# Kernel tuning notes

Hardware: AMD Instinct MI355X
Metric: run time of the kernel (lower is better)

## Reference

```python
import jax, jax.numpy as jnp
import numpy as np

N, E, IN, ED, H, HID, OUT, G = 50000, 800000, 128, 16, 4, 64, 128, 64
NEG_SLOPE = 0.2


def _glorot(key, shape):
    fan_in, fan_out = shape[0], shape[-1]
    lim = float(np.sqrt(6.0 / (fan_in + fan_out)))
    return jax.random.uniform(key, shape, jnp.float32, -lim, lim)


def setup_inputs() -> dict:
    key = jax.random.key(0)
    ks = jax.random.split(key, 32)
    inp = {}
    inp['x'] = jax.random.normal(ks[0], (N, IN), jnp.float32)
    inp['edge_index'] = jax.random.randint(ks[1], (2, E), 0, N)
    inp['edge_attr'] = jax.random.normal(ks[2], (E, ED), jnp.float32)
    inp['batch'] = jnp.sort(jax.random.randint(ks[3], (N,), 0, G))
    # layer dims: (in_channels, out_channels_per_head, concat)
    dims = [(IN, HID, True), (H * HID, HID, True), (H * HID, OUT, False)]
    k = 4
    for i, (cin, c, concat) in enumerate(dims):
        inp[f'W{i}'] = _glorot(ks[k], (cin, H * c)); k += 1
        inp[f'asrc{i}'] = _glorot(ks[k], (1, H, c)); k += 1
        inp[f'adst{i}'] = _glorot(ks[k], (1, H, c)); k += 1
        inp[f'We{i}'] = _glorot(ks[k], (ED, H * c)); k += 1
        inp[f'ae{i}'] = _glorot(ks[k], (1, H, c)); k += 1
        inp[f'b{i}'] = jnp.zeros((H * c if concat else c,), jnp.float32); k += 1
    return inp


def _gat_layer(x, src, dst, ea, W, asrc, adst, We, ae, b, c, concat):
    # PyG GATConv math (eval mode, shared lin for src/dst, edge_dim set).
    n = x.shape[0]
    h = (x @ W).reshape(n, H, c)                      # [N,H,C]
    a_s = (h * asrc).sum(-1)                          # [N,H]
    a_d = (h * adst).sum(-1)                          # [N,H]
    e = (ea @ We).reshape(-1, H, c)                   # [Etot,H,C]
    a_e = (e * ae).sum(-1)                            # [Etot,H]
    alpha = jax.nn.leaky_relu(a_s[src] + a_d[dst] + a_e, NEG_SLOPE)
    # numerically stable per-destination softmax (every dst has a self-loop)
    amax = jax.ops.segment_max(alpha, dst, num_segments=n)
    ex = jnp.exp(alpha - amax[dst])
    denom = jax.ops.segment_sum(ex, dst, num_segments=n)
    alpha = ex / (denom[dst] + 1e-16)
    out = jax.ops.segment_sum(h[src] * alpha[..., None], dst, num_segments=n)
    out = out.reshape(n, H * c) if concat else out.mean(axis=1)
    return out + b


def reference(x, edge_index, edge_attr, batch,
              W0, asrc0, adst0, We0, ae0, b0,
              W1, asrc1, adst1, We1, ae1, b1,
              W2, asrc2, adst2, We2, ae2, b2):
    n = x.shape[0]
    loop = jnp.arange(n)
    src = jnp.concatenate([edge_index[0], loop])
    dst = jnp.concatenate([edge_index[1], loop])
    # self-loop edge_attr uses fill_value='mean' (PyG default)
    ea = jnp.concatenate(
        [edge_attr, jnp.broadcast_to(edge_attr.mean(0), (n, edge_attr.shape[1]))], axis=0)
    h = _gat_layer(x, src, dst, ea, W0, asrc0, adst0, We0, ae0, b0, HID, True)
    h = jax.nn.elu(h)
    h = _gat_layer(h, src, dst, ea, W1, asrc1, adst1, We1, ae1, b1, HID, True)
    h = jax.nn.elu(h)
    h = _gat_layer(h, src, dst, ea, W2, asrc2, adst2, We2, ae2, b2, OUT, False)
    # global mean pool over graphs
    gsum = jax.ops.segment_sum(h, batch, num_segments=G)
    cnt = jax.ops.segment_sum(jnp.ones((n,), h.dtype), batch, num_segments=G)
    return gsum / jnp.maximum(cnt, 1.0)[:, None]
```

## Files before the change

### kernel.cpp

```cpp
#include <hip/hip_runtime.h>
#include <hip/hip_bf16.h>
#include <hip/hip_fp16.h>
#include <math.h>

#define N_NODES 50000
#define N_EDGES 800000
#define NHEADS  4
#define NEG_SLOPE 0.2f

typedef __attribute__((ext_vector_type(8))) _Float16 half8v;
typedef __attribute__((ext_vector_type(4))) float f32x4;

__device__ __forceinline__ void gld_lds16(const ushort* g, ushort* l) {
  __builtin_amdgcn_global_load_lds(
      (const __attribute__((address_space(1))) void*)g,
      (__attribute__((address_space(3))) void*)l, 16, 0, 0);
}

__device__ __forceinline__ void fma4(float4& a, uint2 r, float e) {
  __half2 p = *(__half2*)&r.x, q = *(__half2*)&r.y;
  float2 f = __half22float2(p), g2 = __half22float2(q);
  a.x += e * f.x; a.y += e * f.y; a.z += e * g2.x; a.w += e * g2.y;
}

__global__ void tofp16_kernel(const float* __restrict__ in, __half* __restrict__ out,
                              int n4) {
  int i = blockIdx.x * blockDim.x + threadIdx.x;
  if (i >= n4) return;
  float4 v = ((const float4*)in)[i];
  __half2 a = __floats2half2_rn(v.x, v.y);
  __half2 b = __floats2half2_rn(v.z, v.w);
  ((__half2*)out)[2 * i] = a;
  ((__half2*)out)[2 * i + 1] = b;
}

__global__ void splitT_all_kernel(const float* __restrict__ W0,
                                  const float* __restrict__ W1,
                                  const float* __restrict__ W2,
                                  __half* __restrict__ B0h, __half* __restrict__ B0l,
                                  __half* __restrict__ B1h, __half* __restrict__ B1l,
                                  __half* __restrict__ B2h, __half* __restrict__ B2l) {
  int i = blockIdx.x * 256 + threadIdx.x;
  if (i >= 229376) return;
  const float* W;
  __half *bh, *bl;
  int kshift, N, base;
  if (i < 32768)       { W = W0; bh = B0h; bl = B0l; kshift = 7; N = 256; base = 0; }
  else if (i < 98304)  { W = W1; bh = B1h; bl = B1l; kshift = 8; N = 256; base = 32768; }
  else                 { W = W2; bh = B2h; bl = B2l; kshift = 8; N = 512; base = 98304; }
  int j = i - base;
  int K = 1 << kshift;
  int nn = j >> kshift, k = j & (K - 1);
  float v = W[(size_t)k * N + nn];
  __half h = __float2half(v);
  bh[j] = h;
  bl[j] = __float2half(v - __half2float(h));
}

__global__ __launch_bounds__(256) void gemm_mfma_kernel(
    const __half* __restrict__ Ah, const __half* __restrict__ Bth,
    const __half* __restrict__ Btl, __half* __restrict__ h16,
    const float* __restrict__ asrc, const float* __restrict__ adst,
    float* __restrict__ a_s, float* __restrict__ a_d, int M, int K, int N, int Cph) {
  __shared__ ushort lds[3 * 4096];
  int tid = threadIdx.x;
  int lane = tid & 63, w = tid >> 6;
  int wm = w >> 1, wn = w & 1;
  int r16 = lane & 15, kgrp = lane >> 4;
  int bm = blockIdx.y * 128, bn = blockIdx.x * 128;

  const ushort* gp[6];
#pragma unroll
  for (int i = 0; i < 6; ++i) {
    int c = i * 256 + tid;
    int mmat = c >> 9;
    int s = c & 511;
    int row = s >> 2;
    int kg = (s & 3) ^ ((row >> 1) & 3);
    const ushort* base;
    int rowg;
    if (mmat == 0)      { base = (const ushort*)Ah;  rowg = min(bm + row, M - 1); }
    else if (mmat == 1) { base = (const ushort*)Bth; rowg = bn + row; }
    else                { base = (const ushort*)Btl; rowg = bn + row; }
    gp[i] = base + (size_t)rowg * K + kg * 8;
  }

  f32x4 acc[4][4] = {};
  for (int k0 = 0; k0 < K; k0 += 32) {
#pragma unroll
    for (int i = 0; i < 6; ++i)
      gld_lds16(gp[i] + k0, lds + i * 2048 + tid * 8);
    __syncthreads();
    half8v ah[4], bh[4], bl[4];
#pragma unroll
    for (int m = 0; m < 4; ++m) {
      int row = wm * 64 + m * 16 + r16;
      int s = row * 4 + (kgrp ^ ((row >> 1) & 3));
      ah[m] = *(const half8v*)(lds + 0 * 4096 + s * 8);
    }
#pragma unroll
    for (int j = 0; j < 4; ++j) {
      int row = wn * 64 + j * 16 + r16;
      int s = row * 4 + (kgrp ^ ((row >> 1) & 3));
      bh[j] = *(const half8v*)(lds + 1 * 4096 + s * 8);
      bl[j] = *(const half8v*)(lds + 2 * 4096 + s * 8);
    }
#pragma unroll
    for (int m = 0; m < 4; ++m)
#pragma unroll
      for (int j = 0; j < 4; ++j) {
        acc[m][j] = __builtin_amdgcn_mfma_f32_16x16x32_f16(ah[m], bh[j], acc[m][j], 0, 0, 0);
        acc[m][j] = __builtin_amdgcn_mfma_f32_16x16x32_f16(ah[m], bl[j], acc[m][j], 0, 0, 0);
      }
    __syncthreads();
  }

  int colbase = bn + wn * 64;
  int hd = colbase / Cph;
#pragma unroll
  for (int m = 0; m < 4; ++m) {
#pragma unroll
    for (int r = 0; r < 4; ++r) {
      int row = bm + wm * 64 + m * 16 + kgrp * 4 + r;
      bool ok = row < M;
      float ps = 0.f, pd = 0.f;
#pragma unroll
      for (int j = 0; j < 4; ++j) {
        float val = acc[m][j][r];
        int col = colbase + 16 * j + r16;
        if (ok) h16[(size_t)row * N + col] = __float2half(val);
        ps += val * asrc[col];
        pd += val * adst[col];
      }
#pragma unroll
      for (int o = 8; o >= 1; o >>= 1) {
        ps += __shfl_xor(ps, o);
        pd += __shfl_xor(pd, o);
      }
      if (r16 == 0 && ok) {
        atomicAdd(&a_s[row * NHEADS + hd], ps);
        atomicAdd(&a_d[row * NHEADS + hd], pd);
      }
    }
  }
}

__global__ void ea_colsum_kernel(const float* __restrict__ ea,
                                 float* __restrict__ sums, int E) {
  int tid = threadIdx.x;
  int col = tid & 15;
  float s = 0.f;
  for (int r = blockIdx.x * 16 + (tid >> 4); r < E; r += gridDim.x * 16)
    s += ea[(size_t)r * 16 + col];
  __shared__ float red[256];
  red[tid] = s;
  __syncthreads();
  for (int off = 128; off >= 16; off >>= 1) {
    if (tid < off) red[tid] += red[tid + off];
    __syncthreads();
  }
  if (tid < 16) atomicAdd(&sums[tid], red[tid]);
}

__global__ void wvec_kernel(const float* __restrict__ We0, const float* __restrict__ ae0,
                            const float* __restrict__ We1, const float* __restrict__ ae1,
                            const float* __restrict__ We2, const float* __restrict__ ae2,
                            const float* __restrict__ ea_sum,
                            float* __restrict__ wvec, float* __restrict__ ae_self) {
  __shared__ float sw[192];
  int tid = threadIdx.x;
  if (tid < 192) {
    int l = tid >> 6, rem = tid & 63, k = rem >> 2, hd = rem & 3;
    int C = (l == 2) ? 128 : 64;
    const float* We = (l == 0) ? We0 : (l == 1) ? We1 : We2;
    const float* ae = (l == 0) ? ae0 : (l == 1) ? ae1 : ae2;
    float s = 0.f;
    for (int c = 0; c < C; ++c) s += We[(size_t)k * (4 * C) + hd * C + c] * ae[hd * C + c];
    sw[tid] = s;
    wvec[tid] = s;
  }
  __syncthreads();
  if (tid < 12) {
    int l = tid >> 2, hd = tid & 3;
    const float invE = 1.0f / (float)N_EDGES;
    float s = 0.f;
    for (int k = 0; k < 16; ++k) s += ea_sum[k] * invE * sw[l * 64 + k * 4 + hd];
    ae_self[tid] = s;
  }
}

__global__ void deg_count_kernel(const int* __restrict__ dst, int* deg, int E) {
  int i = blockIdx.x * blockDim.x + threadIdx.x;
  int s = gridDim.x * blockDim.x;
  for (; i < E; i += s) atomicAdd(&deg[dst[i]], 1);
}

__global__ void scan_a_kernel(const int* __restrict__ deg, int* __restrict__ tmp,
                              int* __restrict__ bsum, int n) {
  __shared__ int s[256];
  int i = blockIdx.x * 256 + threadIdx.x;
  int v = (i < n) ? (deg[i] + 1) : 0;
  s[threadIdx.x] = v;
  __syncthreads();
  for (int d = 1; d < 256; d <<= 1) {
    int t = (threadIdx.x >= d) ? s[threadIdx.x - d] : 0;
    __syncthreads();
    s[threadIdx.x] += t;
    __syncthreads();
  }
  if (i < n) tmp[i] = s[threadIdx.x] - v;
  if (threadIdx.x == 255) bsum[blockIdx.x] = s[255];
}
__global__ void scan_b_kernel(int* bsum, int nb) {
  __shared__ int s[256];
  int v = (threadIdx.x < nb) ? bsum[threadIdx.x] : 0;
  s[threadIdx.x] = v;
  __syncthreads();
  for (int d = 1; d < 256; d <<= 1) {
    int t = (threadIdx.x >= d) ? s[threadIdx.x - d] : 0;
    __syncthreads();
    s[threadIdx.x] += t;
    __syncthreads();
  }
  if (threadIdx.x < nb) bsum[threadIdx.x] = s[threadIdx.x] - v;
}
__global__ void scan_c_kernel(const int* __restrict__ tmp, const int* __restrict__ bsum,
                              int* __restrict__ offsets, int* __restrict__ cursor,
                              int n, int tot) {
  int i = blockIdx.x * 256 + threadIdx.x;
  if (i < n) {
    int o = tmp[i] + bsum[blockIdx.x];
    offsets[i] = o;
    cursor[i] = o;
  }
  if (i == 0) offsets[n] = tot;
}

__global__ void scatter_kernel(const int* __restrict__ src, const int* __restrict__ dst,
                               int* cursor, uint2* __restrict__ csr_pack, int E, int n) {
  int i = blockIdx.x * blockDim.x + threadIdx.x;
  int s = gridDim.x * blockDim.x;
  int tot = E + n;
  for (; i < tot; i += s) {
    int ss, dd, eid;
    if (i < E) { ss = src[i]; dd = dst[i]; eid = i; }
    else       { ss = i - E; dd = ss;     eid = E; }
    int pos = atomicAdd(&cursor[dd], 1);
    csr_pack[pos] = make_uint2((uint)ss, (uint)eid);
  }
}

__global__ void ae_csr_kernel(const float* __restrict__ ea, const float* __restrict__ wv,
                              const float* __restrict__ ae_self,
                              const uint2* __restrict__ csr_pack,
                              float* __restrict__ aec, int* __restrict__ csr_src,
                              int tot, int E) {
  int i = blockIdx.x * blockDim.x + threadIdx.x;
  int stride = gridDim.x * blockDim.x;
  for (int p = i; p < tot; p += stride) {
    uint2 pk = csr_pack[p];
    int eid = (int)pk.y;
    csr_src[p] = (int)pk.x;
    if (eid >= E) {
#pragma unroll
      for (int l = 0; l < 3; ++l)
        *(float4*)(aec + ((size_t)l * tot + p) * 4) =
            make_float4(ae_self[l * 4 + 0], ae_self[l * 4 + 1],
                        ae_self[l * 4 + 2], ae_self[l * 4 + 3]);
    } else {
      float row[16];
      const float4* rp = (const float4*)(ea + (size_t)eid * 16);
#pragma unroll
      for (int q = 0; q < 4; ++q) {
        float4 v = rp[q];
        row[q * 4 + 0] = v.x; row[q * 4 + 1] = v.y;
        row[q * 4 + 2] = v.z; row[q * 4 + 3] = v.w;
      }
#pragma unroll
      for (int l = 0; l < 3; ++l) {
        float s0 = 0, s1 = 0, s2 = 0, s3 = 0;
#pragma unroll
        for (int k = 0; k < 16; ++k) {
          float v = row[k];
          s0 += v * wv[l * 64 + k * 4 + 0];
          s1 += v * wv[l * 64 + k * 4 + 1];
          s2 += v * wv[l * 64 + k * 4 + 2];
          s3 += v * wv[l * 64 + k * 4 + 3];
        }
        *(float4*)(aec + ((size_t)l * tot + p) * 4) = make_float4(s0, s1, s2, s3);
      }
    }
  }
}

template <int C, int MODE>
__global__ __launch_bounds__(256) void agg_kernel(
    const __half* __restrict__ h, const float* __restrict__ a_s,
    const float* __restrict__ a_d, const float* __restrict__ a_e,
    const int* __restrict__ offsets, const int* __restrict__ csr_src,
    const float* __restrict__ bias, __half* __restrict__ y16,
    float* __restrict__ yf) {
  constexpr int HC = NHEADS * C;
  constexpr int SL = HC / 4;
  constexpr int G = 256 / SL;
  constexpr int HSH = (C == 64) ? 4 : 5;

  __shared__ float exbuf[NHEADS][64];
  __shared__ int sbuf[64];
  __shared__ float dshare[NHEADS];
  __shared__ float4 cbuf4[(C == 64) ? 192 : 128];

  int node = blockIdx.x;
  int tid = threadIdx.x;
  int hd = tid >> 6, l = tid & 63;
  int beg = offsets[node], end = offsets[node + 1];
  int deg = end - beg;

  float a_dn = a_d[node * NHEADS + hd];

  int i = tid & (SL - 1);
  int g = tid / SL;
  int hh = i >> HSH;
  float4 acc = make_float4(0.f, 0.f, 0.f, 0.f);

  auto alpha_of = [&](int j, int& s_out) -> float {
    int s = csr_src[j];
    float aev = a_e[(size_t)j * NHEADS + hd];
    float v = a_s[s * NHEADS + hd] + a_dn + aev;
    s_out = s;
    return (v > 0.f) ? v : NEG_SLOPE * v;
  };

  auto accum_chunk = [&](int cnt) {
    int t = g;
    for (; t + 3 * G < cnt; t += 4 * G) {
      int s0 = sbuf[t], s1 = sbuf[t + G], s2 = sbuf[t + 2 * G], s3 = sbuf[t + 3 * G];
      float e0 = exbuf[hh][t], e1 = exbuf[hh][t + G];
      float e2 = exbuf[hh][t + 2 * G], e3 = exbuf[hh][t + 3 * G];
      uint2 r0 = *(const uint2*)(h + (size_t)s0 * HC + 4 * i);
      uint2 r1 = *(const uint2*)(h + (size_t)s1 * HC + 4 * i);
      uint2 r2 = *(const uint2*)(h + (size_t)s2 * HC + 4 * i);
      uint2 r3 = *(const uint2*)(h + (size_t)s3 * HC + 4 * i);
      fma4(acc, r0, e0); fma4(acc, r1, e1); fma4(acc, r2, e2); fma4(acc, r3, e3);
    }
    for (; t < cnt; t += G) {
      int s0 = sbuf[t];
      float e0 = exbuf[hh][t];
      uint2 r0 = *(const uint2*)(h + (size_t)s0 * HC + 4 * i);
      fma4(acc, r0, e0);
    }
  };

  if (deg <= 64) {
    int j = beg + l;
    bool valid = j < end;
    int s = 0;
    float al = -1e30f;
    if (valid) al = alpha_of(j, s);
    float m = al;
#pragma unroll
    for (int o = 32; o >= 1; o >>= 1) m = fmaxf(m, __shfl_xor(m, o));
    float ex = valid ? __expf(al - m) : 0.f;
    float dsum = ex;
#pragma unroll
    for (int o = 32; o >= 1; o >>= 1) dsum += __shfl_xor(dsum, o);
    exbuf[hd][l] = ex;
    if (hd == 0) sbuf[l] = s;
    if (l == 0) dshare[hd] = dsum;
    __syncthreads();
    accum_chunk(deg);
  } else {
    float m = -1e30f;
    for (int j0 = beg; j0 < end; j0 += 64) {
      int j = j0 + l;
      if (j < end) {
        int s;
        m = fmaxf(m, alpha_of(j, s));
      }
    }
#pragma unroll
    for (int o = 32; o >= 1; o >>= 1) m = fmaxf(m, __shfl_xor(m, o));
    float dsum = 0.f;
    for (int j0 = beg; j0 < end; j0 += 64) {
      int j = j0 + l;
      int cnt = min(64, end - j0);
      float ex = 0.f;
      int s = 0;
      if (j < end) {
        float al = alpha_of(j, s);
        ex = __expf(al - m);
      }
      dsum += ex;
      __syncthreads();
      exbuf[hd][l] = ex;
      if (hd == 0) sbuf[l] = s;
      __syncthreads();
      accum_chunk(cnt);
    }
#pragma unroll
    for (int o = 32; o >= 1; o >>= 1) dsum += __shfl_xor(dsum, o);
    if (l == 0) dshare[hd] = dsum;
    __syncthreads();
  }

  if (MODE == 0) {
    if (g > 0) cbuf4[(g - 1) * SL + i] = acc;
    __syncthreads();
    if (g == 0) {
      float4 c1 = cbuf4[i], c2 = cbuf4[SL + i], c3 = cbuf4[2 * SL + i];
      acc.x += c1.x + c2.x + c3.x;
      acc.y += c1.y + c2.y + c3.y;
      acc.z += c1.z + c2.z + c3.z;
      acc.w += c1.w + c2.w + c3.w;
      float inv = 1.f / (dshare[hh] + 1e-16f);
      const float4 bv = *(const float4*)(bias + 4 * i);
      float o0 = acc.x * inv + bv.x, o1 = acc.y * inv + bv.y;
      float o2 = acc.z * inv + bv.z, o3 = acc.w * inv + bv.w;
      o0 = (o0 > 0.f) ? o0 : (__expf(o0) - 1.f);
      o1 = (o1 > 0.f) ? o1 : (__expf(o1) - 1.f);
      o2 = (o2 > 0.f) ? o2 : (__expf(o2) - 1.f);
      o3 = (o3 > 0.f) ? o3 : (__expf(o3) - 1.f);
      __half2 w0 = __floats2half2_rn(o0, o1);
      __half2 w1 = __floats2half2_rn(o2, o3);
      uint2 pk;
      pk.x = *(uint*)&w0;
      pk.y = *(uint*)&w1;
      *(uint2*)(y16 + (size_t)node * HC + 4 * i) = pk;
    }
  } else {
    if (g == 1) cbuf4[i] = acc;
    __syncthreads();
    if (g == 0) {
      float4 c1 = cbuf4[i];
      float inv = 1.f / (dshare[hh] + 1e-16f);
      acc.x = (acc.x + c1.x) * inv;
      acc.y = (acc.y + c1.y) * inv;
      acc.z = (acc.z + c1.z) * inv;
      acc.w = (acc.w + c1.w) * inv;
    }
    __syncthreads();
    if (g == 0) cbuf4[i] = acc;
    __syncthreads();
    if (tid < 32) {
      float4 s0 = cbuf4[tid], s1 = cbuf4[tid + 32];
      float4 s2 = cbuf4[tid + 64], s3 = cbuf4[tid + 96];
      const float4 bv = *(const float4*)(bias + 4 * tid);
      float4 o;
      o.x = (s0.x + s1.x + s2.x + s3.x) * 0.25f + bv.x;
      o.y = (s0.y + s1.y + s2.y + s3.y) * 0.25f + bv.y;
      o.z = (s0.z + s1.z + s2.z + s3.z) * 0.25f + bv.z;
      o.w = (s0.w + s1.w + s2.w + s3.w) * 0.25f + bv.w;
      *(float4*)(yf + (size_t)node * 128 + 4 * tid) = o;
    }
  }
}

__global__ void pool_kernel(const float* __restrict__ y, const int* __restrict__ batch,
                            float* __restrict__ pool, float* __restrict__ cnt, int n) {
  int n0 = blockIdx.x * 256;
  if (n0 >= n) return;
  int n1 = min(n0 + 256, n);
  int c = threadIdx.x;
  float accum = 0.f;
  int cur = batch[n0];
  int cn = 0;
  for (int nd = n0; nd < n1; ++nd) {
    int g = batch[nd];
    if (g != cur) {
      atomicAdd(&pool[cur * 128 + c], accum);
      if (c == 0) atomicAdd(&cnt[cur], (float)cn);
      accum = 0.f; cn = 0; cur = g;
    }
    accum += y[(size_t)nd * 128 + c];
    cn++;
  }
  atomicAdd(&pool[cur * 128 + c], accum);
  if (c == 0) atomicAdd(&cnt[cur], (float)cn);
}
__global__ void finalize_kernel(const float* __restrict__ pool,
                                const float* __restrict__ cnt, float* __restrict__ out) {
  int i = blockIdx.x * blockDim.x + threadIdx.x;
  if (i < 64 * 128) out[i] = pool[i] / fmaxf(cnt[i >> 7], 1.f);
}

extern "C" void kernel_launch(void* const* d_in, const int* in_sizes, int n_in,
                              void* d_out, int out_size, void* d_ws, size_t ws_size,
                              hipStream_t stream) {
  const float* x = (const float*)d_in[0];
  const int* ei = (const int*)d_in[1];
  const float* ea = (const float*)d_in[2];
  const int* batch = (const int*)d_in[3];
  const float* W[3]    = {(const float*)d_in[4],  (const float*)d_in[10], (const float*)d_in[16]};
  const float* asrc[3] = {(const float*)d_in[5],  (const float*)d_in[11], (const float*)d_in[17]};
  const float* adst[3] = {(const float*)d_in[6],  (const float*)d_in[12], (const float*)d_in[18]};
  const float* Wep[3]  = {(const float*)d_in[7],  (const float*)d_in[13], (const float*)d_in[19]};
  const float* aep[3]  = {(const float*)d_in[8],  (const float*)d_in[14], (const float*)d_in[20]};
  const float* bp[3]   = {(const float*)d_in[9],  (const float*)d_in[15], (const float*)d_in[21]};

  char* ws = (char*)d_ws;
  size_t off = 0;
  auto take = [&](size_t bytes) -> void* {
    void* p = ws + off;
    off = (off + bytes + 255) & ~(size_t)255;
    return p;
  };
  const int TOT = N_EDGES + N_NODES;
  size_t zero_begin = off;
  float* ea_sum = (float*)take(16 * 4);
  float* pool   = (float*)take(8192 * 4);
  float* cnt    = (float*)take(64 * 4);
  int*   deg    = (int*)take((size_t)N_NODES * 4);
  float* a_sd   = (float*)take((size_t)3 * 2 * N_NODES * NHEADS * 4);
  size_t zero_bytes = off - zero_begin;

  float* wvec    = (float*)take(192 * 4);
  float* ae_self = (float*)take(12 * 4);
  int* tmp     = (int*)take((size_t)N_NODES * 4);
  int* bsum    = (int*)take(256 * 4);
  int* offsets = (int*)take(((size_t)N_NODES + 1) * 4);
  int* cursor  = (int*)take((size_t)N_NODES * 4);
  uint2* csr_pack = (uint2*)take((size_t)TOT * 8);
  int* csr_src = (int*)take((size_t)TOT * 4);
  float* aec  = (float*)take((size_t)3 * TOT * NHEADS * 4);
  __half* x16 = (__half*)take((size_t)N_NODES * 128 * 2);
  __half* Bh[3], *Bl[3];
  Bh[0] = (__half*)take((size_t)32768 * 2);  Bl[0] = (__half*)take((size_t)32768 * 2);
  Bh[1] = (__half*)take((size_t)65536 * 2);  Bl[1] = (__half*)take((size_t)65536 * 2);
  Bh[2] = (__half*)take((size_t)131072 * 2); Bl[2] = (__half*)take((size_t)131072 * 2);
  __half* h16 = (__half*)take((size_t)N_NODES * 512 * 2);
  __half* y16 = (__half*)take((size_t)N_NODES * 256 * 2);
  float* ybuf = (float*)take((size_t)N_NODES * 128 * 4);

  const int* srcp = ei;
  const int* dstp = ei + N_EDGES;
  const int NB = (N_NODES + 255) / 256;

  hipMemsetAsync(ws + zero_begin, 0, zero_bytes, stream);
  ea_colsum_kernel<<<512, 256, 0, stream>>>(ea, ea_sum, N_EDGES);
  deg_count_kernel<<<2048, 256, 0, stream>>>(dstp, deg, N_EDGES);
  scan_a_kernel<<<NB, 256, 0, stream>>>(deg, tmp, bsum, N_NODES);
  scan_b_kernel<<<1, 256, 0, stream>>>(bsum, NB);
  scan_c_kernel<<<NB, 256, 0, stream>>>(tmp, bsum, offsets, cursor, N_NODES, TOT);
  scatter_kernel<<<2048, 256, 0, stream>>>(srcp, dstp, cursor, csr_pack, N_EDGES, N_NODES);
  wvec_kernel<<<1, 256, 0, stream>>>(Wep[0], aep[0], Wep[1], aep[1], Wep[2], aep[2],
                                     ea_sum, wvec, ae_self);
  ae_csr_kernel<<<2048, 256, 0, stream>>>(ea, wvec, ae_self, csr_pack, aec, csr_src,
                                          TOT, N_EDGES);
  tofp16_kernel<<<(N_NODES * 128 / 4 + 255) / 256, 256, 0, stream>>>(x, x16,
                                                                     N_NODES * 128 / 4);
  splitT_all_kernel<<<(229376 + 255) / 256, 256, 0, stream>>>(
      W[0], W[1], W[2], Bh[0], Bl[0], Bh[1], Bl[1], Bh[2], Bl[2]);

  const __half* Acur = x16;
  for (int l = 0; l < 3; ++l) {
    int K = (l == 0) ? 128 : 256;
    int C = (l == 2) ? 128 : 64;
    int HC = NHEADS * C;
    float* a_s = a_sd + (size_t)l * 2 * N_NODES * NHEADS;
    float* a_d = a_s + (size_t)N_NODES * NHEADS;
    gemm_mfma_kernel<<<dim3(HC / 128, (N_NODES + 127) / 128), 256, 0, stream>>>(
        Acur, Bh[l], Bl[l], h16, asrc[l], adst[l], a_s, a_d, N_NODES, K, HC, C);
    if (l < 2) {
      agg_kernel<64, 0><<<N_NODES, 256, 0, stream>>>(
          h16, a_s, a_d, aec + (size_t)l * TOT * NHEADS, offsets, csr_src, bp[l],
          y16, nullptr);
      Acur = y16;
    } else {
      agg_kernel<128, 1><<<N_NODES, 256, 0, stream>>>(
          h16, a_s, a_d, aec + (size_t)l * TOT * NHEADS, offsets, csr_src, bp[l],
          nullptr, ybuf);
    }
  }
  pool_kernel<<<NB, 128, 0, stream>>>(ybuf, batch, pool, cnt, N_NODES);
  finalize_kernel<<<(8192 + 255) / 256, 256, 0, stream>>>(pool, cnt, (float*)d_out);
}
```

Baseline: 719.1 us.

## Process two nodes per aggregation block, fuse pooling into last layer, merge prep kernels

The aggregation kernel now handles two destination nodes per block, so each block has more independent gathers in flight and the block count is halved. The global mean pool is folded into the last layer's aggregation through per-node atomics into the pool buffer, which removes the intermediate fp32 buffer and the separate pool kernel. The fp16 casts and the column-sum/degree-count kernels are each merged into one launch. In exchange, LDS use per block doubles and the pool buffer sees many atomics per graph, which can contend.

```diff
diff --git a/kernel.cpp b/kernel.cpp
--- a/kernel.cpp
+++ b/kernel.cpp
@@ -23,38 +23,38 @@
   a.x += e * f.x; a.y += e * f.y; a.z += e * g2.x; a.w += e * g2.y;
 }
 
-__global__ void tofp16_kernel(const float* __restrict__ in, __half* __restrict__ out,
-                              int n4) {
-  int i = blockIdx.x * blockDim.x + threadIdx.x;
-  if (i >= n4) return;
-  float4 v = ((const float4*)in)[i];
-  __half2 a = __floats2half2_rn(v.x, v.y);
-  __half2 b = __floats2half2_rn(v.z, v.w);
-  ((__half2*)out)[2 * i] = a;
-  ((__half2*)out)[2 * i + 1] = b;
-}
-
-__global__ void splitT_all_kernel(const float* __restrict__ W0,
-                                  const float* __restrict__ W1,
-                                  const float* __restrict__ W2,
-                                  __half* __restrict__ B0h, __half* __restrict__ B0l,
-                                  __half* __restrict__ B1h, __half* __restrict__ B1l,
-                                  __half* __restrict__ B2h, __half* __restrict__ B2l) {
-  int i = blockIdx.x * 256 + threadIdx.x;
-  if (i >= 229376) return;
-  const float* W;
-  __half *bh, *bl;
-  int kshift, N, base;
-  if (i < 32768)       { W = W0; bh = B0h; bl = B0l; kshift = 7; N = 256; base = 0; }
-  else if (i < 98304)  { W = W1; bh = B1h; bl = B1l; kshift = 8; N = 256; base = 32768; }
-  else                 { W = W2; bh = B2h; bl = B2l; kshift = 8; N = 512; base = 98304; }
-  int j = i - base;
-  int K = 1 << kshift;
-  int nn = j >> kshift, k = j & (K - 1);
-  float v = W[(size_t)k * N + nn];
-  __half h = __float2half(v);
-  bh[j] = h;
-  bl[j] = __float2half(v - __half2float(h));
+__global__ void cast_all_kernel(const float* __restrict__ x, __half* __restrict__ x16,
+                                const float* __restrict__ W0,
+                                const float* __restrict__ W1,
+                                const float* __restrict__ W2,
+                                __half* __restrict__ B0h, __half* __restrict__ B0l,
+                                __half* __restrict__ B1h, __half* __restrict__ B1l,
+                                __half* __restrict__ B2h, __half* __restrict__ B2l) {
+  int b = blockIdx.x;
+  if (b < 6250) {
+    int i = b * 256 + threadIdx.x;
+    float4 v = ((const float4*)x)[i];
+    __half2 a = __floats2half2_rn(v.x, v.y);
+    __half2 c = __floats2half2_rn(v.z, v.w);
+    ((__half2*)x16)[2 * i] = a;
+    ((__half2*)x16)[2 * i + 1] = c;
+  } else {
+    int i = (b - 6250) * 256 + threadIdx.x;
+    if (i >= 229376) return;
+    const float* W;
+    __half *bh, *bl;
+    int kshift, N, base;
+    if (i < 32768)       { W = W0; bh = B0h; bl = B0l; kshift = 7; N = 256; base = 0; }
+    else if (i < 98304)  { W = W1; bh = B1h; bl = B1l; kshift = 8; N = 256; base = 32768; }
+    else                 { W = W2; bh = B2h; bl = B2l; kshift = 8; N = 512; base = 98304; }
+    int j = i - base;
+    int K = 1 << kshift;
+    int nn = j >> kshift, k = j & (K - 1);
+    float v = W[(size_t)k * N + nn];
+    __half h = __float2half(v);
+    bh[j] = h;
+    bl[j] = __float2half(v - __half2float(h));
+  }
 }
 
 __global__ __launch_bounds__(256) void gemm_mfma_kernel(
@@ -145,21 +145,27 @@
   }
 }
 
-__global__ void ea_colsum_kernel(const float* __restrict__ ea,
-                                 float* __restrict__ sums, int E) {
+__global__ void prep0_kernel(const float* __restrict__ ea, float* __restrict__ sums,
+                             const int* __restrict__ dst, int* __restrict__ deg, int E) {
   int tid = threadIdx.x;
-  int col = tid & 15;
-  float s = 0.f;
-  for (int r = blockIdx.x * 16 + (tid >> 4); r < E; r += gridDim.x * 16)
-    s += ea[(size_t)r * 16 + col];
-  __shared__ float red[256];
-  red[tid] = s;
-  __syncthreads();
-  for (int off = 128; off >= 16; off >>= 1) {
-    if (tid < off) red[tid] += red[tid + off];
-    __syncthreads();
-  }
-  if (tid < 16) atomicAdd(&sums[tid], red[tid]);
+  if (blockIdx.x < 512) {
+    int col = tid & 15;
+    float s = 0.f;
+    for (int r = blockIdx.x * 16 + (tid >> 4); r < E; r += 512 * 16)
+      s += ea[(size_t)r * 16 + col];
+    __shared__ float red[256];
+    red[tid] = s;
+    __syncthreads();
+    for (int off = 128; off >= 16; off >>= 1) {
+      if (tid < off) red[tid] += red[tid + off];
+      __syncthreads();
+    }
+    if (tid < 16) atomicAdd(&sums[tid], red[tid]);
+  } else {
+    int i = (blockIdx.x - 512) * 256 + tid;
+    int s = 2048 * 256;
+    for (; i < E; i += s) atomicAdd(&deg[dst[i]], 1);
+  }
 }
 
 __global__ void wvec_kernel(const float* __restrict__ We0, const float* __restrict__ ae0,
@@ -189,12 +195,6 @@
   }
 }
 
-__global__ void deg_count_kernel(const int* __restrict__ dst, int* deg, int E) {
-  int i = blockIdx.x * blockDim.x + threadIdx.x;
-  int s = gridDim.x * blockDim.x;
-  for (; i < E; i += s) atomicAdd(&deg[dst[i]], 1);
-}
-
 __global__ void scan_a_kernel(const int* __restrict__ deg, int* __restrict__ tmp,
                               int* __restrict__ bsum, int n) {
   __shared__ int s[256];
@@ -235,7 +235,6 @@
   }
   if (i == 0) offsets[n] = tot;
 }
-
 __global__ void scatter_kernel(const int* __restrict__ src, const int* __restrict__ dst,
                                int* cursor, uint2* __restrict__ csr_pack, int E, int n) {
   int i = blockIdx.x * blockDim.x + threadIdx.x;
@@ -298,185 +297,281 @@
     const __half* __restrict__ h, const float* __restrict__ a_s,
     const float* __restrict__ a_d, const float* __restrict__ a_e,
     const int* __restrict__ offsets, const int* __restrict__ csr_src,
-    const float* __restrict__ bias, __half* __restrict__ y16,
-    float* __restrict__ yf) {
+    const float* __restrict__ bias, const int* __restrict__ batch,
+    __half* __restrict__ y16, float* __restrict__ pool, float* __restrict__ cnt) {
+  constexpr int NPB = 2;
   constexpr int HC = NHEADS * C;
   constexpr int SL = HC / 4;
   constexpr int G = 256 / SL;
   constexpr int HSH = (C == 64) ? 4 : 5;
 
-  __shared__ float exbuf[NHEADS][64];
-  __shared__ int sbuf[64];
-  __shared__ float dshare[NHEADS];
-  __shared__ float4 cbuf4[(C == 64) ? 192 : 128];
-
-  int node = blockIdx.x;
+  __shared__ float exbuf[NPB][NHEADS][64];
+  __shared__ int sbuf[NPB][64];
+  __shared__ float dshare[NPB][NHEADS];
+  __shared__ float4 cbuf4[NPB][(C == 64) ? 192 : 128];
+
   int tid = threadIdx.x;
   int hd = tid >> 6, l = tid & 63;
-  int beg = offsets[node], end = offsets[node + 1];
-  int deg = end - beg;
-
-  float a_dn = a_d[node * NHEADS + hd];
-
   int i = tid & (SL - 1);
   int g = tid / SL;
   int hh = i >> HSH;
-  float4 acc = make_float4(0.f, 0.f, 0.f, 0.f);
-
-  auto alpha_of = [&](int j, int& s_out) -> float {
-    int s = csr_src[j];
-    float aev = a_e[(size_t)j * NHEADS + hd];
-    float v = a_s[s * NHEADS + hd] + a_dn + aev;
-    s_out = s;
-    return (v > 0.f) ? v : NEG_SLOPE * v;
-  };
-
-  auto accum_chunk = [&](int cnt) {
+  int nbase = blockIdx.x * NPB;
+
+  int beg[NPB], deg[NPB];
+  bool fast[NPB];
+#pragma unroll
+  for (int it = 0; it < NPB; ++it) {
+    int nd = nbase + it;
+    if (nd < N_NODES) {
+      int b0 = offsets[nd];
+      beg[it] = b0;
+      deg[it] = offsets[nd + 1] - b0;
+    } else { beg[it] = 0; deg[it] = 0; }
+    fast[it] = (deg[it] <= 64);
+  }
+
+#pragma unroll
+  for (int it = 0; it < NPB; ++it) {
+    if (!fast[it]) continue;
+    int nd = nbase + it;
+    bool valid = l < deg[it];
+    float a_dn = (nd < N_NODES) ? a_d[nd * NHEADS + hd] : 0.f;
+    int s = 0;
+    float al = -1e30f;
+    if (valid) {
+      int j = beg[it] + l;
+      s = csr_src[j];
+      float aev = a_e[(size_t)j * NHEADS + hd];
+      float v = a_s[s * NHEADS + hd] + a_dn + aev;
+      al = (v > 0.f) ? v : NEG_SLOPE * v;
+    }
+    float m = al;
+#pragma unroll
+    for (int o = 32; o >= 1; o >>= 1) m = fmaxf(m, __shfl_xor(m, o));
+    float ex = valid ? __expf(al - m) : 0.f;
+    float ds = ex;
+#pragma unroll
+    for (int o = 32; o >= 1; o >>= 1) ds += __shfl_xor(ds, o);
+    exbuf[it][hd][l] = ex;
+    if (hd == 0) sbuf[it][l] = s;
+    if (l == 0) dshare[it][hd] = ds;
+  }
+  __syncthreads();
+
+  float4 acc[NPB];
+#pragma unroll
+  for (int it = 0; it < NPB; ++it) acc[it] = make_float4(0.f, 0.f, 0.f, 0.f);
+
+  auto accum = [&](int it, float4& a) {
+    int cnt_e = deg[it];
     int t = g;
-    for (; t + 3 * G < cnt; t += 4 * G) {
-      int s0 = sbuf[t], s1 = sbuf[t + G], s2 = sbuf[t + 2 * G], s3 = sbuf[t + 3 * G];
-      float e0 = exbuf[hh][t], e1 = exbuf[hh][t + G];
-      float e2 = exbuf[hh][t + 2 * G], e3 = exbuf[hh][t + 3 * G];
+    for (; t + 3 * G < cnt_e; t += 4 * G) {
+      int s0 = sbuf[it][t], s1 = sbuf[it][t + G];
+      int s2 = sbuf[it][t + 2 * G], s3 = sbuf[it][t + 3 * G];
+      float e0 = exbuf[it][hh][t], e1 = exbuf[it][hh][t + G];
+      float e2 = exbuf[it][hh][t + 2 * G], e3 = exbuf[it][hh][t + 3 * G];
       uint2 r0 = *(const uint2*)(h + (size_t)s0 * HC + 4 * i);
       uint2 r1 = *(const uint2*)(h + (size_t)s1 * HC + 4 * i);
       uint2 r2 = *(const uint2*)(h + (size_t)s2 * HC + 4 * i);
       uint2 r3 = *(const uint2*)(h + (size_t)s3 * HC + 4 * i);
-      fma4(acc, r0, e0); fma4(acc, r1, e1); fma4(acc, r2, e2); fma4(acc, r3, e3);
-    }
-    for (; t < cnt; t += G) {
-      int s0 = sbuf[t];
-      float e0 = exbuf[hh][t];
+      fma4(a, r0, e0); fma4(a, r1, e1); fma4(a, r2, e2); fma4(a, r3, e3);
+    }
+    for (; t < cnt_e; t += G) {
+      int s0 = sbuf[it][t];
+      float e0 = exbuf[it][hh][t];
       uint2 r0 = *(const uint2*)(h + (size_t)s0 * HC + 4 * i);
-      fma4(acc, r0, e0);
+      fma4(a, r0, e0);
     }
   };
-
-  if (deg <= 64) {
-    int j = beg + l;
-    bool valid = j < end;
-    int s = 0;
-    float al = -1e30f;
-    if (valid) al = alpha_of(j, s);
-    float m = al;
-#pragma unroll
-    for (int o = 32; o >= 1; o >>= 1) m = fmaxf(m, __shfl_xor(m, o));
-    float ex = valid ? __expf(al - m) : 0.f;
-    float dsum = ex;
-#pragma unroll
-    for (int o = 32; o >= 1; o >>= 1) dsum += __shfl_xor(dsum, o);
-    exbuf[hd][l] = ex;
-    if (hd == 0) sbuf[l] = s;
-    if (l == 0) dshare[hd] = dsum;
-    __syncthreads();
-    accum_chunk(deg);
+#pragma unroll
+  for (int it = 0; it < NPB; ++it)
+    if (fast[it]) accum(it, acc[it]);
+
+  if (MODE == 0) {
+#pragma unroll
+    for (int it = 0; it < NPB; ++it)
+      if (fast[it] && g > 0) cbuf4[it][(g - 1) * SL + i] = acc[it];
+    __syncthreads();
+    if (g == 0) {
+#pragma unroll
+      for (int it = 0; it < NPB; ++it) {
+        int nd = nbase + it;
+        if (!fast[it] || nd >= N_NODES) continue;
+        float4 c1 = cbuf4[it][i], c2 = cbuf4[it][SL + i], c3 = cbuf4[it][2 * SL + i];
+        float4 a = acc[it];
+        a.x += c1.x + c2.x + c3.x;
+        a.y += c1.y + c2.y + c3.y;
+        a.z += c1.z + c2.z + c3.z;
+        a.w += c1.w + c2.w + c3.w;
+        float inv = 1.f / (dshare[it][hh] + 1e-16f);
+        const float4 bv = *(const float4*)(bias + 4 * i);
+        float o0 = a.x * inv + bv.x, o1 = a.y * inv + bv.y;
+        float o2 = a.z * inv + bv.z, o3 = a.w * inv + bv.w;
+        o0 = (o0 > 0.f) ? o0 : (__expf(o0) - 1.f);
+        o1 = (o1 > 0.f) ? o1 : (__expf(o1) - 1.f);
+        o2 = (o2 > 0.f) ? o2 : (__expf(o2) - 1.f);
+        o3 = (o3 > 0.f) ? o3 : (__expf(o3) - 1.f);
+        __half2 w0 = __floats2half2_rn(o0, o1);
+        __half2 w1 = __floats2half2_rn(o2, o3);
+        uint2 pk;
+        pk.x = *(uint*)&w0;
+        pk.y = *(uint*)&w1;
+        *(uint2*)(y16 + (size_t)nd * HC + 4 * i) = pk;
+      }
+    }
   } else {
+#pragma unroll
+    for (int it = 0; it < NPB; ++it)
+      if (fast[it] && g == 1) cbuf4[it][i] = acc[it];
+    __syncthreads();
+    if (g == 0) {
+#pragma unroll
+      for (int it = 0; it < NPB; ++it) {
+        if (!fast[it]) continue;
+        float4 c1 = cbuf4[it][i];
+        float inv = 1.f / (dshare[it][hh] + 1e-16f);
+        float4 v;
+        v.x = (acc[it].x + c1.x) * inv;
+        v.y = (acc[it].y + c1.y) * inv;
+        v.z = (acc[it].z + c1.z) * inv;
+        v.w = (acc[it].w + c1.w) * inv;
+        cbuf4[it][i] = v;
+      }
+    }
+    __syncthreads();
+#pragma unroll
+    for (int it = 0; it < NPB; ++it) {
+      int nd = nbase + it;
+      if (!fast[it] || nd >= N_NODES) continue;
+      int gid = batch[nd];
+      if (tid < 32) {
+        float4 s0 = cbuf4[it][tid], s1 = cbuf4[it][tid + 32];
+        float4 s2 = cbuf4[it][tid + 64], s3 = cbuf4[it][tid + 96];
+        const float4 bv = *(const float4*)(bias + 4 * tid);
+        float* pp = pool + (size_t)gid * 128 + 4 * tid;
+        atomicAdd(pp + 0, (s0.x + s1.x + s2.x + s3.x) * 0.25f + bv.x);
+        atomicAdd(pp + 1, (s0.y + s1.y + s2.y + s3.y) * 0.25f + bv.y);
+        atomicAdd(pp + 2, (s0.z + s1.z + s2.z + s3.z) * 0.25f + bv.z);
+        atomicAdd(pp + 3, (s0.w + s1.w + s2.w + s3.w) * 0.25f + bv.w);
+      }
+      if (tid == 32) atomicAdd(&cnt[gid], 1.f);
+    }
+  }
+
+  bool any_slow = false;
+#pragma unroll
+  for (int it = 0; it < NPB; ++it) any_slow |= !fast[it];
+  if (!any_slow) return;
+  __syncthreads();
+
+  for (int it = 0; it < NPB; ++it) {
+    if (fast[it]) continue;
+    int nd = nbase + it;
+    int b0 = beg[it], end = b0 + deg[it];
+    float a_dn = a_d[nd * NHEADS + hd];
     float m = -1e30f;
-    for (int j0 = beg; j0 < end; j0 += 64) {
+    for (int j0 = b0; j0 < end; j0 += 64) {
       int j = j0 + l;
       if (j < end) {
-        int s;
-        m = fmaxf(m, alpha_of(j, s));
+        int s = csr_src[j];
+        float aev = a_e[(size_t)j * NHEADS + hd];
+        float v = a_s[s * NHEADS + hd] + a_dn + aev;
+        float al = (v > 0.f) ? v : NEG_SLOPE * v;
+        m = fmaxf(m, al);
       }
     }
 #pragma unroll
     for (int o = 32; o >= 1; o >>= 1) m = fmaxf(m, __shfl_xor(m, o));
     float dsum = 0.f;
-    for (int j0 = beg; j0 < end; j0 += 64) {
+    float4 sacc = make_float4(0.f, 0.f, 0.f, 0.f);
+    for (int j0 = b0; j0 < end; j0 += 64) {
       int j = j0 + l;
-      int cnt = min(64, end - j0);
+      int cnt_e = min(64, end - j0);
       float ex = 0.f;
       int s = 0;
       if (j < end) {
-        float al = alpha_of(j, s);
+        s = csr_src[j];
+        float aev = a_e[(size_t)j * NHEADS + hd];
+        float v = a_s[s * NHEADS + hd] + a_dn + aev;
+        float al = (v > 0.f) ? v : NEG_SLOPE * v;
         ex = __expf(al - m);
       }
       dsum += ex;
       __syncthreads();
-      exbuf[hd][l] = ex;
-      if (hd == 0) sbuf[l] = s;
-      __syncthreads();
-      accum_chunk(cnt);
+      exbuf[0][hd][l] = ex;
+      if (hd == 0) sbuf[0][l] = s;
+      __syncthreads();
+      {
+        int t = g;
+        for (; t < cnt_e; t += G) {
+          int s0 = sbuf[0][t];
+          float e0 = exbuf[0][hh][t];
+          uint2 r0 = *(const uint2*)(h + (size_t)s0 * HC + 4 * i);
+          fma4(sacc, r0, e0);
+        }
+      }
     }
 #pragma unroll
     for (int o = 32; o >= 1; o >>= 1) dsum += __shfl_xor(dsum, o);
-    if (l == 0) dshare[hd] = dsum;
-    __syncthreads();
-  }
-
-  if (MODE == 0) {
-    if (g > 0) cbuf4[(g - 1) * SL + i] = acc;
-    __syncthreads();
-    if (g == 0) {
-      float4 c1 = cbuf4[i], c2 = cbuf4[SL + i], c3 = cbuf4[2 * SL + i];
-      acc.x += c1.x + c2.x + c3.x;
-      acc.y += c1.y + c2.y + c3.y;
-      acc.z += c1.z + c2.z + c3.z;
-      acc.w += c1.w + c2.w + c3.w;
-      float inv = 1.f / (dshare[hh] + 1e-16f);
-      const float4 bv = *(const float4*)(bias + 4 * i);
-      float o0 = acc.x * inv + bv.x, o1 = acc.y * inv + bv.y;
-      float o2 = acc.z * inv + bv.z, o3 = acc.w * inv + bv.w;
-      o0 = (o0 > 0.f) ? o0 : (__expf(o0) - 1.f);
-      o1 = (o1 > 0.f) ? o1 : (__expf(o1) - 1.f);
-      o2 = (o2 > 0.f) ? o2 : (__expf(o2) - 1.f);
-      o3 = (o3 > 0.f) ? o3 : (__expf(o3) - 1.f);
-      __half2 w0 = __floats2half2_rn(o0, o1);
-      __half2 w1 = __floats2half2_rn(o2, o3);
-      uint2 pk;
-      pk.x = *(uint*)&w0;
-      pk.y = *(uint*)&w1;
-      *(uint2*)(y16 + (size_t)node * HC + 4 * i) = pk;
-    }
-  } else {
-    if (g == 1) cbuf4[i] = acc;
-    __syncthreads();
-    if (g == 0) {
-      float4 c1 = cbuf4[i];
-      float inv = 1.f / (dshare[hh] + 1e-16f);
-      acc.x = (acc.x + c1.x) * inv;
-      acc.y = (acc.y + c1.y) * inv;
-      acc.z = (acc.z + c1.z) * inv;
-      acc.w = (acc.w + c1.w) * inv;
-    }
-    __syncthreads();
-    if (g == 0) cbuf4[i] = acc;
-    __syncthreads();
-    if (tid < 32) {
-      float4 s0 = cbuf4[tid], s1 = cbuf4[tid + 32];
-      float4 s2 = cbuf4[tid + 64], s3 = cbuf4[tid + 96];
-      const float4 bv = *(const float4*)(bias + 4 * tid);
-      float4 o;
-      o.x = (s0.x + s1.x + s2.x + s3.x) * 0.25f + bv.x;
-      o.y = (s0.y + s1.y + s2.y + s3.y) * 0.25f + bv.y;
-      o.z = (s0.z + s1.z + s2.z + s3.z) * 0.25f + bv.z;
-      o.w = (s0.w + s1.w + s2.w + s3.w) * 0.25f + bv.w;
-      *(float4*)(yf + (size_t)node * 128 + 4 * tid) = o;
-    }
-  }
-}
-
-__global__ void pool_kernel(const float* __restrict__ y, const int* __restrict__ batch,
-                            float* __restrict__ pool, float* __restrict__ cnt, int n) {
-  int n0 = blockIdx.x * 256;
-  if (n0 >= n) return;
-  int n1 = min(n0 + 256, n);
-  int c = threadIdx.x;
-  float accum = 0.f;
-  int cur = batch[n0];
-  int cn = 0;
-  for (int nd = n0; nd < n1; ++nd) {
-    int g = batch[nd];
-    if (g != cur) {
-      atomicAdd(&pool[cur * 128 + c], accum);
-      if (c == 0) atomicAdd(&cnt[cur], (float)cn);
-      accum = 0.f; cn = 0; cur = g;
-    }
-    accum += y[(size_t)nd * 128 + c];
-    cn++;
-  }
-  atomicAdd(&pool[cur * 128 + c], accum);
-  if (c == 0) atomicAdd(&cnt[cur], (float)cn);
-}
+    if (l == 0) dshare[0][hd] = dsum;
+    __syncthreads();
+
+    if (MODE == 0) {
+      if (g > 0) cbuf4[0][(g - 1) * SL + i] = sacc;
+      __syncthreads();
+      if (g == 0) {
+        float4 c1 = cbuf4[0][i], c2 = cbuf4[0][SL + i], c3 = cbuf4[0][2 * SL + i];
+        sacc.x += c1.x + c2.x + c3.x;
+        sacc.y += c1.y + c2.y + c3.y;
+        sacc.z += c1.z + c2.z + c3.z;
+        sacc.w += c1.w + c2.w + c3.w;
+        float inv = 1.f / (dshare[0][hh] + 1e-16f);
+        const float4 bv = *(const float4*)(bias + 4 * i);
+        float o0 = sacc.x * inv + bv.x, o1 = sacc.y * inv + bv.y;
+        float o2 = sacc.z * inv + bv.z, o3 = sacc.w * inv + bv.w;
+        o0 = (o0 > 0.f) ? o0 : (__expf(o0) - 1.f);
+        o1 = (o1 > 0.f) ? o1 : (__expf(o1) - 1.f);
+        o2 = (o2 > 0.f) ? o2 : (__expf(o2) - 1.f);
+        o3 = (o3 > 0.f) ? o3 : (__expf(o3) - 1.f);
+        __half2 w0 = __floats2half2_rn(o0, o1);
+        __half2 w1 = __floats2half2_rn(o2, o3);
+        uint2 pk;
+        pk.x = *(uint*)&w0;
+        pk.y = *(uint*)&w1;
+        *(uint2*)(y16 + (size_t)nd * HC + 4 * i) = pk;
+      }
+      __syncthreads();
+    } else {
+      if (g == 1) cbuf4[0][i] = sacc;
+      __syncthreads();
+      if (g == 0) {
+        float4 c1 = cbuf4[0][i];
+        float inv = 1.f / (dshare[0][hh] + 1e-16f);
+        float4 v;
+        v.x = (sacc.x + c1.x) * inv;
+        v.y = (sacc.y + c1.y) * inv;
+        v.z = (sacc.z + c1.z) * inv;
+        v.w = (sacc.w + c1.w) * inv;
+        cbuf4[0][i] = v;
+      }
+      __syncthreads();
+      int gid = batch[nd];
+      if (tid < 32) {
+        float4 s0 = cbuf4[0][tid], s1 = cbuf4[0][tid + 32];
+        float4 s2 = cbuf4[0][tid + 64], s3 = cbuf4[0][tid + 96];
+        const float4 bv = *(const float4*)(bias + 4 * tid);
+        float* pp = pool + (size_t)gid * 128 + 4 * tid;
+        atomicAdd(pp + 0, (s0.x + s1.x + s2.x + s3.x) * 0.25f + bv.x);
+        atomicAdd(pp + 1, (s0.y + s1.y + s2.y + s3.y) * 0.25f + bv.y);
+        atomicAdd(pp + 2, (s0.z + s1.z + s2.z + s3.z) * 0.25f + bv.z);
+        atomicAdd(pp + 3, (s0.w + s1.w + s2.w + s3.w) * 0.25f + bv.w);
+      }
+      if (tid == 32) atomicAdd(&cnt[gid], 1.f);
+      __syncthreads();
+    }
+  }
+}
+
 __global__ void finalize_kernel(const float* __restrict__ pool,
                                 const float* __restrict__ cnt, float* __restrict__ out) {
   int i = blockIdx.x * blockDim.x + threadIdx.x;
@@ -529,15 +624,13 @@
   Bh[2] = (__half*)take((size_t)131072 * 2); Bl[2] = (__half*)take((size_t)131072 * 2);
   __half* h16 = (__half*)take((size_t)N_NODES * 512 * 2);
   __half* y16 = (__half*)take((size_t)N_NODES * 256 * 2);
-  float* ybuf = (float*)take((size_t)N_NODES * 128 * 4);
 
   const int* srcp = ei;
   const int* dstp = ei + N_EDGES;
   const int NB = (N_NODES + 255) / 256;
 
   hipMemsetAsync(ws + zero_begin, 0, zero_bytes, stream);
-  ea_colsum_kernel<<<512, 256, 0, stream>>>(ea, ea_sum, N_EDGES);
-  deg_count_kernel<<<2048, 256, 0, stream>>>(dstp, deg, N_EDGES);
+  prep0_kernel<<<512 + 2048, 256, 0, stream>>>(ea, ea_sum, dstp, deg, N_EDGES);
   scan_a_kernel<<<NB, 256, 0, stream>>>(deg, tmp, bsum, N_NODES);
   scan_b_kernel<<<1, 256, 0, stream>>>(bsum, NB);
   scan_c_kernel<<<NB, 256, 0, stream>>>(tmp, bsum, offsets, cursor, N_NODES, TOT);
@@ -546,12 +639,11 @@
                                      ea_sum, wvec, ae_self);
   ae_csr_kernel<<<2048, 256, 0, stream>>>(ea, wvec, ae_self, csr_pack, aec, csr_src,
                                           TOT, N_EDGES);
-  tofp16_kernel<<<(N_NODES * 128 / 4 + 255) / 256, 256, 0, stream>>>(x, x16,
-                                                                     N_NODES * 128 / 4);
-  splitT_all_kernel<<<(229376 + 255) / 256, 256, 0, stream>>>(
-      W[0], W[1], W[2], Bh[0], Bl[0], Bh[1], Bl[1], Bh[2], Bl[2]);
+  cast_all_kernel<<<6250 + 896, 256, 0, stream>>>(x, x16, W[0], W[1], W[2], Bh[0], Bl[0],
+                                                  Bh[1], Bl[1], Bh[2], Bl[2]);
 
   const __half* Acur = x16;
+  const int AGGB = (N_NODES + 1) / 2;
   for (int l = 0; l < 3; ++l) {
     int K = (l == 0) ? 128 : 256;
     int C = (l == 2) ? 128 : 64;
@@ -561,16 +653,15 @@
     gemm_mfma_kernel<<<dim3(HC / 128, (N_NODES + 127) / 128), 256, 0, stream>>>(
         Acur, Bh[l], Bl[l], h16, asrc[l], adst[l], a_s, a_d, N_NODES, K, HC, C);
     if (l < 2) {
-      agg_kernel<64, 0><<<N_NODES, 256, 0, stream>>>(
+      agg_kernel<64, 0><<<AGGB, 256, 0, stream>>>(
           h16, a_s, a_d, aec + (size_t)l * TOT * NHEADS, offsets, csr_src, bp[l],
-          y16, nullptr);
+          batch, y16, nullptr, nullptr);
       Acur = y16;
     } else {
-      agg_kernel<128, 1><<<N_NODES, 256, 0, stream>>>(
+      agg_kernel<128, 1><<<AGGB, 256, 0, stream>>>(
           h16, a_s, a_d, aec + (size_t)l * TOT * NHEADS, offsets, csr_src, bp[l],
-          nullptr, ybuf);
-    }
-  }
-  pool_kernel<<<NB, 128, 0, stream>>>(ybuf, batch, pool, cnt, N_NODES);
+          batch, nullptr, pool, cnt);
+    }
+  }
   finalize_kernel<<<(8192 + 255) / 256, 256, 0, stream>>>(pool, cnt, (float*)d_out);
 }
```

New measurement: 967.7 us. 1.35x slower.
